# Kernel tuning notes

Hardware: AMD Instinct MI355X
Metric: run time of the kernel (lower is better)

## Reference

```python
import jax, jax.numpy as jnp
import numpy as np

B, N, FIN = 64, 128, 768
NFEAT, NHID, NHEADS, NCLASS = 1024, 512, 8, 512
ALPHA = 0.2
NEG_E = -9e15
NEG_S = -9e10


def setup_inputs():
    rng = np.random.RandomState(0)
    x = rng.randn(B, N, FIN).astype(np.float32)
    offset_mapping = np.zeros((B, N, 2), dtype=np.int32)
    attention_mask = np.zeros((B, N), dtype=np.float32)
    tag = np.zeros((B, N), dtype=np.float32)
    for b in range(B):
        pos, k, groups = 1, 0, 0
        n_words = int(rng.randint(30, 60))
        for _ in range(n_words):
            wl = int(rng.randint(1, 4))
            if k + wl > 120:
                break
            for _t in range(wl):
                offset_mapping[b, k] = (pos, pos + 2)  # contiguous inside word
                pos += 2
                k += 1
            pos += 1  # 1-char gap => word boundary: end == next_start - 1
            groups += 1
        groups -= 1  # last word is never closed (matches torch loop semantics)
        attention_mask[b, :groups] = 1.0
        tag[b, :groups] = (rng.rand(groups) > 0.1).astype(np.float32)
        tag[b, 0] = 1.0
    adj = (rng.rand(B, N, N) < 0.3).astype(np.float32)
    adj = np.clip(adj + np.eye(N, dtype=np.float32)[None], 0.0, 1.0)
    s = 0.02
    p = {
        'Wg_w': s * rng.randn(FIN, NFEAT), 'Wg_b': np.zeros(NFEAT),
        'hW_w': s * rng.randn(NHEADS, NFEAT, NHID), 'hW_b': np.zeros((NHEADS, NHID)),
        'ha_w': s * rng.randn(NHEADS, 2 * NHID), 'ha_b': np.zeros(NHEADS),
        'oW_w': s * rng.randn(NHID * NHEADS, NCLASS), 'oW_b': np.zeros(NCLASS),
        'oa_w': s * rng.randn(2 * NCLASS), 'oa_b': np.zeros(()),
        'fin_w': s * rng.randn(NCLASS, 1), 'fin_b': np.zeros(1),
    }
    inp = {
        'x': jnp.asarray(x), 'tag': jnp.asarray(tag),
        'offset_mapping': jnp.asarray(offset_mapping),
        'attention_mask': jnp.asarray(attention_mask), 'adj': jnp.asarray(adj),
    }
    for kk, vv in p.items():
        inp[kk] = jnp.asarray(np.asarray(vv, dtype=np.float32))
    return inp


def _group_pool(x, offs):
    # Vectorized form of the offset-grouped mean pooling loop.
    zero = (offs[:, :, 0] == 0) & (offs[:, :, 1] == 0)  # padding rows
    fz = jnp.argmax(zero, axis=1)                       # first padding row (break)
    pos = jnp.arange(N)
    valid = pos[None, :] < fz[:, None]
    nxt_start = jnp.concatenate([offs[:, 1:, 0], jnp.zeros((offs.shape[0], 1), offs.dtype)], axis=1)
    boundary = valid & (offs[:, :, 1] == nxt_start - 1)
    bi = boundary.astype(jnp.int32)
    cs = jnp.cumsum(bi, axis=1)
    seg = cs - bi                 # exclusive cumsum: group id per token
    G = cs[:, -1]                 # number of closed groups per row

    def per(xb, segb, bb):
        sums = jax.ops.segment_sum(xb, segb, num_segments=N + 1)[:N]
        cnts = jax.ops.segment_sum(jnp.ones((N,), xb.dtype), segb, num_segments=N + 1)[:N]
        ends = jax.ops.segment_sum((jnp.arange(N) + 1) * bb, segb, num_segments=N + 1)[:N]
        return sums, cnts, ends

    sums, cnts, ends = jax.vmap(per)(x, seg, bi)
    g = jnp.arange(N)[None, :]
    gv = g < G[:, None]
    x_off = jnp.where(gv[..., None], sums / jnp.maximum(cnts, 1.0)[..., None], 0.0)
    starts = jnp.concatenate([jnp.zeros((offs.shape[0], 1), jnp.int32), ends[:, :-1]], axis=1)
    starts = jnp.where(gv, starts, 0)
    ends = jnp.where(gv, ends, 0)
    return x_off, jnp.stack([starts, ends], axis=-1)  # [B,N,F_in], [B,N,2]


def _expand_row(fix):
    # Flatten [start,end) ranges in order until the first [0,0] row; rest = arange.
    zr = (fix[:, 0] == 0) & (fix[:, 1] == 0)
    fz = jnp.argmax(zr)
    valid = jnp.arange(N) < fz
    lens = jnp.where(valid, fix[:, 1] - fix[:, 0], 0)
    csum = jnp.cumsum(lens)
    excl = csum - lens
    total = csum[-1]
    l = jnp.arange(N)
    k = jnp.clip(jnp.searchsorted(csum, l, side='right'), 0, N - 1)
    val = fix[k, 0] + (l - excl[k])
    return jnp.where(l < total, val, l)


def _scores(x_off, tag, attention_mask, adj, Wg_w, Wg_b, hW_w, hW_b, ha_w, ha_b, oW_w, oW_b, oa_w, oa_b, fin_w, fin_b):
    xw = x_off @ Wg_w + Wg_b                                    # [B,N,NFEAT]
    h = jnp.einsum('bnf,hfo->bhno', xw, hW_w) + hW_b[None, :, None, :]
    # e_ij = leakyrelu(a1.h_i + a2.h_j + b): decomposition of a([h_i||h_j])
    e = jax.nn.leaky_relu(
        jnp.einsum('bhno,ho->bhn', h, ha_w[:, :NHID])[:, :, :, None]
        + jnp.einsum('bhno,ho->bhn', h, ha_w[:, NHID:])[:, :, None, :]
        + ha_b[None, :, None, None], ALPHA)
    att = jax.nn.softmax(jnp.where(adj[:, None, :, :] > 0, e, NEG_E), axis=-1)
    x1 = jax.nn.elu(jnp.einsum('bhij,bhjo->bhio', att, h))
    x1 = x1.transpose(0, 2, 1, 3).reshape(x1.shape[0], N, NHEADS * NHID)
    h2 = x1 @ oW_w + oW_b
    e2 = jax.nn.leaky_relu((h2 @ oa_w[:NCLASS])[:, :, None]
                           + (h2 @ oa_w[NCLASS:])[:, None, :] + oa_b, ALPHA)
    att2 = jax.nn.softmax(jnp.where(adj > 0, e2, NEG_E), axis=-1)
    x2 = jax.nn.elu(jnp.einsum('bij,bjo->bio', att2, h2))
    logits = (x2 @ fin_w + fin_b)[..., 0]                        # [B,N]
    m = jnp.where(tag > 0, attention_mask, 0.0)
    sc = jax.nn.softmax(jnp.where(m > 0, logits * m, NEG_S), axis=1)
    summary = m.sum(axis=1)
    ii = (jnp.arange(N, 0, -1).astype(jnp.float32)[None, :] / summary[:, None]) * m
    ii = jax.nn.softmax(jnp.where(m > 0, ii, NEG_S), axis=1)
    return sc + ii


def reference(x, tag, offset_mapping, attention_mask, adj, Wg_w, Wg_b, hW_w, hW_b, ha_w, ha_b, oW_w, oW_b, oa_w, oa_b, fin_w, fin_b):
    x_off, index_group = _group_pool(x, offset_mapping)
    sc = _scores(x_off, tag, attention_mask, adj, Wg_w, Wg_b, hW_w, hW_b, ha_w, ha_b, oW_w, oW_b, oa_w, oa_b, fin_w, fin_b)
    order = jnp.argsort(-sc, axis=1)  # jax argsort is stable; matches torch stable descending
    bidx = jnp.arange(sc.shape[0])[:, None]
    fix = index_group.at[bidx, order].set(index_group)  # scatter_(dim=1) with permutation index
    return jax.vmap(_expand_row)(fix)
```

## Files before the change

### kernel.cpp

```cpp
#include <hip/hip_runtime.h>
#include <cstddef>
#include <cstdint>

#define B_ 64
#define N_ 128
#define FIN_ 768
#define NEG_E_ (-9.0e15f)
#define NEG_S_ (-9.0e10f)
#define CHUNK_ 16

typedef unsigned short u16;
typedef unsigned int u32;
typedef float f32x4 __attribute__((ext_vector_type(4)));
typedef short s16x8 __attribute__((ext_vector_type(8)));
typedef u16 u16x4 __attribute__((ext_vector_type(4)));

__device__ __forceinline__ u16 f2bf(float x) {
  u32 u = __float_as_uint(x);
  return (u16)((u + 0x7fffu + ((u >> 16) & 1u)) >> 16);
}
__device__ __forceinline__ float b2f(u16 h) {
  return __uint_as_float(((u32)h) << 16);
}

__global__ __launch_bounds__(128) void group_pool_kernel(
    const float* __restrict__ x, const int* __restrict__ offs,
    u16* __restrict__ xoh, u16* __restrict__ xol, int* __restrict__ ig)
{
  const int b = blockIdx.x;
  const int fc = blockIdx.y;
  const int tid = threadIdx.x;
  __shared__ int o0[N_], o1[N_];
  __shared__ int bnd[N_];
  __shared__ float invlen[N_];
  __shared__ int st[N_], en[N_];
  __shared__ int Gs;
  o0[tid] = offs[(b * N_ + tid) * 2 + 0];
  o1[tid] = offs[(b * N_ + tid) * 2 + 1];
  bnd[tid] = -1;
  __syncthreads();
  if (tid == 0) {
    int fz = N_;
    for (int k = 0; k < N_; ++k) { if (o0[k] == 0 && o1[k] == 0) { fz = k; break; } }
    int g = 0, prev = 0;
    for (int k = 0; k < fz; ++k) {
      int nxt = (k + 1 < N_) ? o0[k + 1] : 0;
      if (o1[k] == nxt - 1 && g < N_) {
        bnd[k] = g;
        invlen[g] = 1.0f / (float)(k + 1 - prev);
        st[g] = prev;
        en[g] = k + 1;
        prev = k + 1;
        ++g;
      }
    }
    Gs = g;
  }
  __syncthreads();
  const int G = Gs;
  const int f = fc * 128 + tid;
  const float* xb = x + (size_t)b * N_ * FIN_ + f;
  float acc = 0.0f;
  for (int k0 = 0; k0 < N_; k0 += 8) {
    float v[8];
#pragma unroll
    for (int u = 0; u < 8; ++u) v[u] = xb[(size_t)(k0 + u) * FIN_];
#pragma unroll
    for (int u = 0; u < 8; ++u) {
      acc += v[u];
      int g = bnd[k0 + u];
      if (g >= 0) {
        float mean = acc * invlen[g];
        u16 hh = f2bf(mean);
        size_t oo = ((size_t)b * N_ + g) * FIN_ + f;
        xoh[oo] = hh;
        xol[oo] = f2bf(mean - b2f(hh));
        acc = 0.0f;
      }
    }
  }
  for (int g = G; g < N_; ++g) {
    size_t oo = ((size_t)b * N_ + g) * FIN_ + f;
    xoh[oo] = 0;
    xol[oo] = 0;
  }
  if (fc == 0) {
    int g = tid;
    ig[(b * N_ + g) * 2 + 0] = (g < G) ? st[g] : 0;
    ig[(b * N_ + g) * 2 + 1] = (g < G) ? en[g] : 0;
  }
}

__global__ __launch_bounds__(256) void pack_wgT(
    const float* __restrict__ w, u16* __restrict__ th, u16* __restrict__ tl)
{
  __shared__ float t[32][33];
  const int k0 = blockIdx.x * 32, n0 = blockIdx.y * 32;
  const int r = threadIdx.x >> 3;
  const int c = (threadIdx.x & 7) * 4;
  float4 v = *(const float4*)(w + (size_t)(k0 + r) * 1024 + n0 + c);
  t[r][c] = v.x; t[r][c + 1] = v.y; t[r][c + 2] = v.z; t[r][c + 3] = v.w;
  __syncthreads();
  u16x4 hv, lv;
#pragma unroll
  for (int i = 0; i < 4; ++i) {
    float xv = t[c + i][r];
    u16 h = f2bf(xv);
    hv[i] = h; lv[i] = f2bf(xv - b2f(h));
  }
  size_t dst = (size_t)(n0 + r) * 768 + k0 + c;
  *(u16x4*)(th + dst) = hv;
  *(u16x4*)(tl + dst) = lv;
}
__global__ __launch_bounds__(256) void pack_hwT(
    const float* __restrict__ w, u16* __restrict__ th, u16* __restrict__ tl)
{
  __shared__ float t[32][33];
  const int o0 = blockIdx.x * 32, f0 = blockIdx.y * 32, hd = blockIdx.z;
  const int r = threadIdx.x >> 3;
  const int c = (threadIdx.x & 7) * 4;
  float4 v = *(const float4*)(w + ((size_t)hd * 1024 + f0 + r) * 512 + o0 + c);
  t[r][c] = v.x; t[r][c + 1] = v.y; t[r][c + 2] = v.z; t[r][c + 3] = v.w;
  __syncthreads();
  u16x4 hv, lv;
#pragma unroll
  for (int i = 0; i < 4; ++i) {
    float xv = t[c + i][r];
    u16 h = f2bf(xv);
    hv[i] = h; lv[i] = f2bf(xv - b2f(h));
  }
  size_t dst = ((size_t)hd * 512 + o0 + r) * 1024 + f0 + c;
  *(u16x4*)(th + dst) = hv;
  *(u16x4*)(tl + dst) = lv;
}
__global__ __launch_bounds__(256) void pack_owT(
    const float* __restrict__ w, u16* __restrict__ th, u16* __restrict__ tl)
{
  __shared__ float t[32][33];
  const int k0 = blockIdx.x * 32, o0 = blockIdx.y * 32;
  const int r = threadIdx.x >> 3;
  const int c = (threadIdx.x & 7) * 4;
  float4 v = *(const float4*)(w + (size_t)(k0 + r) * 512 + o0 + c);
  t[r][c] = v.x; t[r][c + 1] = v.y; t[r][c + 2] = v.z; t[r][c + 3] = v.w;
  __syncthreads();
  u16x4 hv, lv;
#pragma unroll
  for (int i = 0; i < 4; ++i) {
    float xv = t[c + i][r];
    u16 h = f2bf(xv);
    hv[i] = h; lv[i] = f2bf(xv - b2f(h));
  }
  size_t dst = (size_t)(o0 + r) * 4096 + k0 + c;
  *(u16x4*)(th + dst) = hv;
  *(u16x4*)(tl + dst) = lv;
}

__global__ __launch_bounds__(256) void mfma_split_gemm(
    const u16* __restrict__ Ah, const u16* __restrict__ Al,
    const u16* __restrict__ Bh, const u16* __restrict__ Bl,
    const float* __restrict__ bias, int bias_mode,
    u16* __restrict__ Oh, u16* __restrict__ Ol, float* __restrict__ Of,
    int out_f32, int do_elu,
    int K, int lda, int ldb,
    long long Az, long long Bz,
    int msh, long long s_mb, int nsh, long long s_nb, long long s_n,
    long long zb_s, long long zh_s, int zH)
{
  __shared__ u16 As_h[128][40];
  __shared__ u16 As_l[128][40];
  __shared__ u16 Bs_h[128][40];
  __shared__ u16 Bs_l[128][40];
  const int tid = threadIdx.x;
  const int wave = tid >> 6, lane = tid & 63;
  const int wm = (wave >> 1) * 64, wn = (wave & 1) * 64;
  const int bn = blockIdx.x * 128, bm = blockIdx.y * 128;
  const int z = blockIdx.z;
  const u16* Ahb = Ah + (long long)z * Az;
  const u16* Alb = Al + (long long)z * Az;
  const u16* Bhb = Bh + (long long)z * Bz;
  const u16* Blb = Bl + (long long)z * Bz;
  const int lm = lane & 15, lq = lane >> 4;

  const int sr = tid >> 1;
  const int sc = (tid & 1) * 16;
  const size_t ga = (size_t)(bm + sr) * lda + sc;
  const size_t gb = (size_t)(bn + sr) * ldb + sc;

  f32x4 acc[4][4];
#pragma unroll
  for (int i = 0; i < 4; ++i)
#pragma unroll
    for (int j = 0; j < 4; ++j) acc[i][j] = (f32x4){0.0f, 0.0f, 0.0f, 0.0f};

  uint4 r0, r1, r2, r3, r4, r5, r6, r7;
  r0 = *(const uint4*)(Ahb + ga);
  r1 = *(const uint4*)(Ahb + ga + 8);
  r2 = *(const uint4*)(Alb + ga);
  r3 = *(const uint4*)(Alb + ga + 8);
  r4 = *(const uint4*)(Bhb + gb);
  r5 = *(const uint4*)(Bhb + gb + 8);
  r6 = *(const uint4*)(Blb + gb);
  r7 = *(const uint4*)(Blb + gb + 8);

  for (int k0 = 0; k0 < K; k0 += 32) {
    __syncthreads();
    *(uint4*)&As_h[sr][sc] = r0;
    *(uint4*)&As_h[sr][sc + 8] = r1;
    *(uint4*)&As_l[sr][sc] = r2;
    *(uint4*)&As_l[sr][sc + 8] = r3;
    *(uint4*)&Bs_h[sr][sc] = r4;
    *(uint4*)&Bs_h[sr][sc + 8] = r5;
    *(uint4*)&Bs_l[sr][sc] = r6;
    *(uint4*)&Bs_l[sr][sc + 8] = r7;
    __syncthreads();
    int kn = k0 + 32;
    if (kn < K) {
      r0 = *(const uint4*)(Ahb + ga + kn);
      r1 = *(const uint4*)(Ahb + ga + kn + 8);
      r2 = *(const uint4*)(Alb + ga + kn);
      r3 = *(const uint4*)(Alb + ga + kn + 8);
      r4 = *(const uint4*)(Bhb + gb + kn);
      r5 = *(const uint4*)(Bhb + gb + kn + 8);
      r6 = *(const uint4*)(Blb + gb + kn);
      r7 = *(const uint4*)(Blb + gb + kn + 8);
    }
    s16x8 fa_h[4], fa_l[4], fb_h[4], fb_l[4];
#pragma unroll
    for (int t = 0; t < 4; ++t) {
      fa_h[t] = *(const s16x8*)&As_h[wm + t * 16 + lm][lq * 8];
      fa_l[t] = *(const s16x8*)&As_l[wm + t * 16 + lm][lq * 8];
      fb_h[t] = *(const s16x8*)&Bs_h[wn + t * 16 + lm][lq * 8];
      fb_l[t] = *(const s16x8*)&Bs_l[wn + t * 16 + lm][lq * 8];
    }
#pragma unroll
    for (int i = 0; i < 4; ++i)
#pragma unroll
      for (int j = 0; j < 4; ++j) {
        acc[i][j] = __builtin_amdgcn_mfma_f32_16x16x32_bf16(fa_h[i], fb_h[j], acc[i][j], 0, 0, 0);
        acc[i][j] = __builtin_amdgcn_mfma_f32_16x16x32_bf16(fa_h[i], fb_l[j], acc[i][j], 0, 0, 0);
        acc[i][j] = __builtin_amdgcn_mfma_f32_16x16x32_bf16(fa_l[i], fb_h[j], acc[i][j], 0, 0, 0);
      }
  }

  __syncthreads();
  const long long zoff = (long long)(z / zH) * zb_s + (long long)(z % zH) * zh_s;
  const int mmask = (1 << msh) - 1;
  const int nmask = (1 << nsh) - 1;
  char* lds_raw = (char*)&As_h[0][0] + wave * 4608;
  const int rn = lane >> 2;
  const int rm = (lane & 3) * 16;

  if (out_f32) {
    float* slab = (float*)lds_raw;
#pragma unroll
    for (int j = 0; j < 4; ++j) {
#pragma unroll
      for (int i = 0; i < 4; ++i) {
        int mb = bm + wm + i * 16 + lq * 4;
        int n = bn + wn + j * 16 + lm;
        f32x4 v = acc[i][j];
        if (bias_mode == 1) v += bias[n];
        else if (bias_mode == 2) { f32x4 b4 = *(const f32x4*)&bias[mb]; v += b4; }
        if (do_elu) {
          v.x = v.x > 0.0f ? v.x : expm1f(v.x);
          v.y = v.y > 0.0f ? v.y : expm1f(v.y);
          v.z = v.z > 0.0f ? v.z : expm1f(v.z);
          v.w = v.w > 0.0f ? v.w : expm1f(v.w);
        }
        *(f32x4*)&slab[lm * 68 + i * 16 + lq * 4] = v;
      }
      __syncthreads();
      int n = bn + wn + j * 16 + rn;
      int mbase = bm + wm + rm;
      long long off = (long long)(mbase >> msh) * s_mb + (mbase & mmask)
                    + (long long)(n >> nsh) * s_nb + (long long)(n & nmask) * s_n + zoff;
      const float* src = &slab[rn * 68 + rm];
      f32x4 v0 = *(const f32x4*)(src + 0);
      f32x4 v1 = *(const f32x4*)(src + 4);
      f32x4 v2 = *(const f32x4*)(src + 8);
      f32x4 v3 = *(const f32x4*)(src + 12);
      *(f32x4*)(Of + off + 0)  = v0;
      *(f32x4*)(Of + off + 4)  = v1;
      *(f32x4*)(Of + off + 8)  = v2;
      *(f32x4*)(Of + off + 12) = v3;
      __syncthreads();
    }
  } else {
    u16* slab_h = (u16*)lds_raw;
    u16* slab_l = slab_h + 16 * 72;
#pragma unroll
    for (int j = 0; j < 4; ++j) {
#pragma unroll
      for (int i = 0; i < 4; ++i) {
        int mb = bm + wm + i * 16 + lq * 4;
        int n = bn + wn + j * 16 + lm;
        f32x4 v = acc[i][j];
        if (bias_mode == 1) v += bias[n];
        else if (bias_mode == 2) { f32x4 b4 = *(const f32x4*)&bias[mb]; v += b4; }
        if (do_elu) {
          v.x = v.x > 0.0f ? v.x : expm1f(v.x);
          v.y = v.y > 0.0f ? v.y : expm1f(v.y);
          v.z = v.z > 0.0f ? v.z : expm1f(v.z);
          v.w = v.w > 0.0f ? v.w : expm1f(v.w);
        }
        u16 h0 = f2bf(v.x), h1 = f2bf(v.y), h2 = f2bf(v.z), h3 = f2bf(v.w);
        u16x4 hv = {h0, h1, h2, h3};
        u16x4 lv = {f2bf(v.x - b2f(h0)), f2bf(v.y - b2f(h1)),
                    f2bf(v.z - b2f(h2)), f2bf(v.w - b2f(h3))};
        *(u16x4*)&slab_h[lm * 72 + i * 16 + lq * 4] = hv;
        *(u16x4*)&slab_l[lm * 72 + i * 16 + lq * 4] = lv;
      }
      __syncthreads();
      int n = bn + wn + j * 16 + rn;
      int mbase = bm + wm + rm;
      long long off = (long long)(mbase >> msh) * s_mb + (mbase & mmask)
                    + (long long)(n >> nsh) * s_nb + (long long)(n & nmask) * s_n + zoff;
      const u16* sh = &slab_h[rn * 72 + rm];
      const u16* sl = &slab_l[rn * 72 + rm];
      uint4 h0 = *(const uint4*)(sh + 0);
      uint4 h1 = *(const uint4*)(sh + 8);
      uint4 l0 = *(const uint4*)(sl + 0);
      uint4 l1 = *(const uint4*)(sl + 8);
      *(uint4*)(Oh + off + 0) = h0;
      *(uint4*)(Oh + off + 8) = h1;
      *(uint4*)(Ol + off + 0) = l0;
      *(uint4*)(Ol + off + 8) = l1;
      __syncthreads();
    }
  }
}

#define G8_BUF 49152

#define STAGE_A8(T) do { const int _t = (T); if (_t < nt) {                    \
    const int _q = _t % 3;                                                     \
    _Pragma("unroll")                                                          \
    for (int rg_ = 0; rg_ < 2; ++rg_)                                          \
      __builtin_amdgcn_global_load_lds(                                        \
          (const __attribute__((address_space(1))) void*)(gA +                 \
              (size_t)_t * 32 + (size_t)rg_ * 8 * lda),                        \
          (__attribute__((address_space(3))) void*)(ldsAd + _q * G8_BUF +      \
              rg_ * 1024),                                                     \
          16, 0, 0);                                                           \
  } } while (0)

#define STAGE_B8(T) do { const int _t = (T); if (_t < nt) {                    \
    const int _q = _t % 3;                                                     \
    _Pragma("unroll")                                                          \
    for (int rg_ = 0; rg_ < 4; ++rg_)                                          \
      __builtin_amdgcn_global_load_lds(                                        \
          (const __attribute__((address_space(1))) void*)(gB +                 \
              (size_t)_t * 32 + (size_t)rg_ * 8 * ldb),                        \
          (__attribute__((address_space(3))) void*)(ldsBd + _q * G8_BUF +      \
              rg_ * 1024),                                                     \
          16, 0, 0);                                                           \
  } } while (0)

__global__ __launch_bounds__(512, 2) void mfma_split_gemm8(
    const u16* __restrict__ Ah, const u16* __restrict__ Al,
    const u16* __restrict__ Bh, const u16* __restrict__ Bl,
    const float* __restrict__ bias, int bias_mode,
    u16* __restrict__ Oh, u16* __restrict__ Ol,
    int K, int lda, int ldb,
    int msh, long long s_mb, int nsh, long long s_nb, long long s_n)
{
  __shared__ __align__(128) char ldsb[3 * G8_BUF];
  const int tid = threadIdx.x;
  const int wave = tid >> 6, lane = tid & 63;
  const int wm = (wave >> 2) * 64, wn = (wave & 3) * 64;
  const int bn = blockIdx.x * 256, bm = blockIdx.y * 128;
  const int lm = lane & 15, lq = lane >> 4;
  const int nt = K >> 5;

  const int srow = lane >> 3;
  const int sl = (lane & 7) ^ srow;
  const int scol = (sl & 3) * 8;
  const u16* Asel = (sl < 4) ? Ah : Al;
  const u16* Bsel = (sl < 4) ? Bh : Bl;

  const u16* gA = Asel + (size_t)(bm + wave * 16 + srow) * lda + scol;
  const u16* gB = Bsel + (size_t)(bn + wave * 32 + srow) * ldb + scol;
  char* ldsAd = ldsb + wave * 2048;
  char* ldsBd = ldsb + 16384 + wave * 4096;

  const int hbyt = (lq ^ (lm & 7)) * 16;
  const int lbyt = hbyt ^ 64;

  f32x4 acc[4][4];
#pragma unroll
  for (int i = 0; i < 4; ++i)
#pragma unroll
    for (int j = 0; j < 4; ++j) acc[i][j] = (f32x4){0.0f, 0.0f, 0.0f, 0.0f};

  STAGE_A8(0); STAGE_B8(0);
  STAGE_A8(1); STAGE_B8(1);
  if (nt > 1) asm volatile("s_waitcnt vmcnt(6)" ::: "memory");
  else        asm volatile("s_waitcnt vmcnt(0)" ::: "memory");
  __builtin_amdgcn_s_barrier();
  __builtin_amdgcn_sched_barrier(0);

#pragma unroll 3
  for (int t = 0; t < nt; ++t) {
    const int q = t % 3;
    STAGE_A8(t + 2);
    STAGE_B8(t + 2);
    const char* Abase = ldsb + q * G8_BUF + (wm + lm) * 128;
    const char* Bbase = ldsb + q * G8_BUF + 16384 + (wn + lm) * 128;
    s16x8 fa[4][2], fb[4][2];
#pragma unroll
    for (int i = 0; i < 4; ++i) {
      fb[i][0] = *(const s16x8*)(Bbase + i * 2048 + hbyt);
      fb[i][1] = *(const s16x8*)(Bbase + i * 2048 + lbyt);
      fa[i][0] = *(const s16x8*)(Abase + i * 2048 + hbyt);
      fa[i][1] = *(const s16x8*)(Abase + i * 2048 + lbyt);
    }
    __builtin_amdgcn_s_setprio(1);
#pragma unroll
    for (int i = 0; i < 4; ++i)
#pragma unroll
      for (int j = 0; j < 4; ++j) {
        acc[i][j] = __builtin_amdgcn_mfma_f32_16x16x32_bf16(fa[i][0], fb[j][0], acc[i][j], 0, 0, 0);
        acc[i][j] = __builtin_amdgcn_mfma_f32_16x16x32_bf16(fa[i][0], fb[j][1], acc[i][j], 0, 0, 0);
        acc[i][j] = __builtin_amdgcn_mfma_f32_16x16x32_bf16(fa[i][1], fb[j][0], acc[i][j], 0, 0, 0);
      }
    __builtin_amdgcn_s_setprio(0);
    if (t + 1 < nt) {
      if (t + 2 < nt) asm volatile("s_waitcnt vmcnt(6)" ::: "memory");
      else            asm volatile("s_waitcnt vmcnt(0)" ::: "memory");
      __builtin_amdgcn_s_barrier();
      __builtin_amdgcn_sched_barrier(0);
    }
  }

  __syncthreads();
  const int mmask = (1 << msh) - 1;
  const int nmask = (1 << nsh) - 1;
  char* lds_raw = ldsb + wave * 4608;
  const int rn = lane >> 2;
  const int rm = (lane & 3) * 16;
  u16* slab_h = (u16*)lds_raw;
  u16* slab_l = slab_h + 16 * 72;
#pragma unroll
  for (int j = 0; j < 4; ++j) {
#pragma unroll
    for (int i = 0; i < 4; ++i) {
      int mb = bm + wm + i * 16 + lq * 4;
      int n = bn + wn + j * 16 + lm;
      f32x4 v = acc[i][j];
      if (bias_mode == 1) v += bias[n];
      else if (bias_mode == 2) { f32x4 b4 = *(const f32x4*)&bias[mb]; v += b4; }
      u16 h0 = f2bf(v.x), h1 = f2bf(v.y), h2 = f2bf(v.z), h3 = f2bf(v.w);
      u16x4 hv = {h0, h1, h2, h3};
      u16x4 lv = {f2bf(v.x - b2f(h0)), f2bf(v.y - b2f(h1)),
                  f2bf(v.z - b2f(h2)), f2bf(v.w - b2f(h3))};
      *(u16x4*)&slab_h[lm * 72 + i * 16 + lq * 4] = hv;
      *(u16x4*)&slab_l[lm * 72 + i * 16 + lq * 4] = lv;
    }
    __syncthreads();
    int n = bn + wn + j * 16 + rn;
    int mbase = bm + wm + rm;
    long long off = (long long)(mbase >> msh) * s_mb + (mbase & mmask)
                  + (long long)(n >> nsh) * s_nb + (long long)(n & nmask) * s_n;
    const u16* sh = &slab_h[rn * 72 + rm];
    const u16* slp = &slab_l[rn * 72 + rm];
    uint4 h0 = *(const uint4*)(sh + 0);
    uint4 h1 = *(const uint4*)(sh + 8);
    uint4 l0 = *(const uint4*)(slp + 0);
    uint4 l1 = *(const uint4*)(slp + 8);
    *(uint4*)(Oh + off + 0) = h0;
    *(uint4*)(Oh + off + 8) = h1;
    *(uint4*)(Ol + off + 0) = l0;
    *(uint4*)(Ol + off + 8) = l1;
    __syncthreads();
  }
}

__global__ __launch_bounds__(256) void reduce4_bias(
    const float* __restrict__ ps, const float* __restrict__ bias,
    float* __restrict__ h2T, int col0)
{
  int base = (blockIdx.x * 256 + threadIdx.x) * 4;
  int o = base >> 11, m = base & 2047;
  f32x4 v = *(const f32x4*)(ps + base);
  v += *(const f32x4*)(ps + base + 1048576);
  v += *(const f32x4*)(ps + base + 2097152);
  v += *(const f32x4*)(ps + base + 3145728);
  v += bias[o];
  *(f32x4*)(h2T + (size_t)o * 8192 + col0 + m) = v;
}

__global__ __launch_bounds__(512) void dot_pairs_hT(
    const u16* __restrict__ hTh, const u16* __restrict__ hTl,
    const float* __restrict__ W,
    float* __restrict__ esrc, float* __restrict__ edst)
{
  int bh = blockIdx.x;
  int head = bh & 7;
  int tid = threadIdx.x;
  int os = tid >> 7, i = tid & 127;
  const u16* ph = hTh + (size_t)bh * 65536 + (size_t)os * 16384 + i;
  const u16* pl = hTl + (size_t)bh * 65536 + (size_t)os * 16384 + i;
  const float* w1 = W + head * 1024 + os * 128;
  float s1 = 0.0f, s2 = 0.0f;
#pragma unroll 8
  for (int o = 0; o < 128; ++o) {
    float hv = b2f(ph[o * 128]) + b2f(pl[o * 128]);
    s1 = fmaf(hv, w1[o], s1);
    s2 = fmaf(hv, w1[512 + o], s2);
  }
  __shared__ float sh1[4][128], sh2[4][128];
  sh1[os][i] = s1;
  sh2[os][i] = s2;
  __syncthreads();
  if (os == 0) {
    esrc[bh * 128 + i] = sh1[0][i] + sh1[1][i] + sh1[2][i] + sh1[3][i];
    edst[bh * 128 + i] = sh2[0][i] + sh2[1][i] + sh2[2][i] + sh2[3][i];
  }
}

__global__ __launch_bounds__(512) void dot_pairs_h2T(
    const float* __restrict__ h2T, const float* __restrict__ oa,
    float* __restrict__ e2s, float* __restrict__ e2d)
{
  int b = blockIdx.x;
  int tid = threadIdx.x;
  int os = tid >> 7, i = tid & 127;
  const float* hb = h2T + (size_t)os * 128 * 8192 + b * 128 + i;
  const float* oa1 = oa + os * 128;
  float s1 = 0.0f, s2 = 0.0f;
#pragma unroll 8
  for (int o = 0; o < 128; ++o) {
    float hv = hb[(size_t)o * 8192];
    s1 = fmaf(hv, oa1[o], s1);
    s2 = fmaf(hv, oa1[512 + o], s2);
  }
  __shared__ float sh1[4][128], sh2[4][128];
  sh1[os][i] = s1;
  sh2[os][i] = s2;
  __syncthreads();
  if (os == 0) {
    e2s[b * 128 + i] = sh1[0][i] + sh1[1][i] + sh1[2][i] + sh1[3][i];
    e2d[b * 128 + i] = sh2[0][i] + sh2[1][i] + sh2[2][i] + sh2[3][i];
  }
}

__global__ __launch_bounds__(64) void edge_softmax_kernel(
    const float* __restrict__ esrc, const float* __restrict__ edst,
    const float* __restrict__ bias, const float* __restrict__ adj,
    float* __restrict__ attf, u16* __restrict__ atth, u16* __restrict__ attl,
    int H, int split)
{
  int row = blockIdx.x;
  int lane = threadIdx.x;
  int i = row & 127;
  int bh = row >> 7;
  int hd = bh % H;
  int b = bh / H;
  float es = esrc[row] + bias[hd];
  const float* adjr = adj + ((size_t)b * N_ + i) * N_;
  const float* edr = edst + (size_t)bh * N_;
  float v[2];
#pragma unroll
  for (int t = 0; t < 2; ++t) {
    int j = lane + t * 64;
    float e = es + edr[j];
    e = (e >= 0.0f) ? e : 0.2f * e;
    v[t] = (adjr[j] > 0.0f) ? e : NEG_E_;
  }
  float mx = fmaxf(v[0], v[1]);
  for (int off = 32; off; off >>= 1) mx = fmaxf(mx, __shfl_xor(mx, off));
  float e0 = expf(v[0] - mx), e1 = expf(v[1] - mx);
  float sm = e0 + e1;
  for (int off = 32; off; off >>= 1) sm += __shfl_xor(sm, off);
  float inv = 1.0f / sm;
  float p0 = e0 * inv, p1 = e1 * inv;
  size_t base = (size_t)row * N_;
  if (split) {
    u16 h0 = f2bf(p0), h1 = f2bf(p1);
    atth[base + lane] = h0;
    attl[base + lane] = f2bf(p0 - b2f(h0));
    atth[base + lane + 64] = h1;
    attl[base + lane + 64] = f2bf(p1 - b2f(h1));
  } else {
    attf[base + lane] = p0;
    attf[base + lane + 64] = p1;
  }
}

__global__ __launch_bounds__(256) void bgemm_elu_bt_f32(
    const float* __restrict__ A, const float* __restrict__ BT,
    float* __restrict__ C)
{
  __shared__ float As[16][64];
  __shared__ float Bs[16][68];
  const int tid = threadIdx.x;
  const int tm = blockIdx.x >> 3, tn = blockIdx.x & 7;
  const int bm = tm * 64, bn = tn * 64;
  const int b = blockIdx.y;
  const float* Ab = A + (size_t)b * 16384;
  const float* BTb = BT + (size_t)b * 128;
  const int ty = tid >> 4, tx = tid & 15;
  const int ar = tid >> 2, ac = (tid & 3) * 4;
  float acc[4][4];
#pragma unroll
  for (int i = 0; i < 4; ++i)
#pragma unroll
    for (int j = 0; j < 4; ++j) acc[i][j] = 0.0f;

  for (int k0 = 0; k0 < 128; k0 += 16) {
    float4 av = *(const float4*)(Ab + (size_t)(bm + ar) * 128 + k0 + ac);
    float4 bv = *(const float4*)(BTb + (size_t)(bn + ar) * 8192 + k0 + ac);
    __syncthreads();
    As[ac + 0][ar] = av.x; As[ac + 1][ar] = av.y; As[ac + 2][ar] = av.z; As[ac + 3][ar] = av.w;
    Bs[ac + 0][ar] = bv.x; Bs[ac + 1][ar] = bv.y; Bs[ac + 2][ar] = bv.z; Bs[ac + 3][ar] = bv.w;
    __syncthreads();
#pragma unroll
    for (int kk = 0; kk < 16; ++kk) {
      float a[4], bb[4];
      *(float4*)a  = *(const float4*)&As[kk][ty * 4];
      *(float4*)bb = *(const float4*)&Bs[kk][tx * 4];
#pragma unroll
      for (int i = 0; i < 4; ++i)
#pragma unroll
        for (int j = 0; j < 4; ++j)
          acc[i][j] = fmaf(a[i], bb[j], acc[i][j]);
    }
  }
#pragma unroll
  for (int i = 0; i < 4; ++i) {
    int row = b * 128 + bm + ty * 4 + i;
    float4 v;
    v.x = acc[i][0] > 0.0f ? acc[i][0] : expm1f(acc[i][0]);
    v.y = acc[i][1] > 0.0f ? acc[i][1] : expm1f(acc[i][1]);
    v.z = acc[i][2] > 0.0f ? acc[i][2] : expm1f(acc[i][2]);
    v.w = acc[i][3] > 0.0f ? acc[i][3] : expm1f(acc[i][3]);
    *(float4*)(C + (size_t)row * 512 + bn + tx * 4) = v;
  }
}

__global__ __launch_bounds__(256) void logits_kernel(
    const float* __restrict__ X, const float* __restrict__ w,
    const float* __restrict__ bptr, float* __restrict__ out, int R)
{
  int wv = (blockIdx.x * 256 + threadIdx.x) >> 6;
  int lane = threadIdx.x & 63;
  if (wv >= R) return;
  const float* xr = X + (size_t)wv * 512;
  float s = 0.0f;
#pragma unroll
  for (int i = 0; i < 8; ++i) {
    int c = lane + i * 64;
    s = fmaf(xr[c], w[c], s);
  }
  for (int off = 32; off; off >>= 1) s += __shfl_down(s, off);
  if (lane == 0) out[wv] = s + bptr[0];
}

__global__ __launch_bounds__(128) void finalize_kernel(
    const float* __restrict__ logits, const float* __restrict__ tag,
    const float* __restrict__ amask, const int* __restrict__ ig,
    int* __restrict__ out)
{
  const int b = blockIdx.x, tid = threadIdx.x;
  __shared__ float red[N_];
  __shared__ float scs[N_];
  __shared__ int fs[N_], fe[N_], lens[N_], csum[N_];
  __shared__ int redi[N_];

  float lg = logits[b * N_ + tid];
  float tg = tag[b * N_ + tid];
  float am = amask[b * N_ + tid];
  float m = (tg > 0.0f) ? am : 0.0f;

  float in1 = (m > 0.0f) ? lg * m : NEG_S_;
  red[tid] = in1; __syncthreads();
  for (int s = 64; s > 0; s >>= 1) { if (tid < s) red[tid] = fmaxf(red[tid], red[tid + s]); __syncthreads(); }
  float M1 = red[0]; __syncthreads();
  float e1 = expf(in1 - M1);
  red[tid] = e1; __syncthreads();
  for (int s = 64; s > 0; s >>= 1) { if (tid < s) red[tid] += red[tid + s]; __syncthreads(); }
  float S1 = red[0]; __syncthreads();
  float sc = e1 / S1;

  red[tid] = m; __syncthreads();
  for (int s = 64; s > 0; s >>= 1) { if (tid < s) red[tid] += red[tid + s]; __syncthreads(); }
  float SM = red[0]; __syncthreads();

  float in2 = (m > 0.0f) ? ((float)(N_ - tid) / SM) * m : NEG_S_;
  red[tid] = in2; __syncthreads();
  for (int s = 64; s > 0; s >>= 1) { if (tid < s) red[tid] = fmaxf(red[tid], red[tid + s]); __syncthreads(); }
  float M2 = red[0]; __syncthreads();
  float e2 = expf(in2 - M2);
  red[tid] = e2; __syncthreads();
  for (int s = 64; s > 0; s >>= 1) { if (tid < s) red[tid] += red[tid + s]; __syncthreads(); }
  float S2 = red[0]; __syncthreads();
  float ii = e2 / S2;

  scs[tid] = sc + ii;
  __syncthreads();

  float si = scs[tid];
  int rank = 0;
  for (int j = 0; j < N_; ++j) {
    float sj = scs[j];
    rank += (sj > si) || (sj == si && j < tid);
  }
  fs[tid] = ig[(b * N_ + rank) * 2 + 0];
  fe[tid] = ig[(b * N_ + rank) * 2 + 1];
  __syncthreads();

  redi[tid] = (fs[tid] == 0 && fe[tid] == 0) ? tid : N_;
  __syncthreads();
  for (int s = 64; s > 0; s >>= 1) { if (tid < s) redi[tid] = min(redi[tid], redi[tid + s]); __syncthreads(); }
  int fz = redi[0]; __syncthreads();
  lens[tid] = (tid < fz) ? (fe[tid] - fs[tid]) : 0;
  __syncthreads();
  if (tid == 0) {
    int r = 0;
    for (int k = 0; k < N_; ++k) { r += lens[k]; csum[k] = r; }
  }
  __syncthreads();
  int total = csum[N_ - 1];
  int l = tid;
  int k = 0;
  while (k < N_ && csum[k] <= l) ++k;
  if (k > N_ - 1) k = N_ - 1;
  int val = fs[k] + (l - (csum[k] - lens[k]));
  out[b * N_ + l] = (l < total) ? val : l;
}

extern "C" void kernel_launch(void* const* d_in, const int* in_sizes, int n_in,
                              void* d_out, int out_size, void* d_ws, size_t ws_size,
                              hipStream_t stream)
{
  const float* x     = (const float*)d_in[0];
  const float* tag   = (const float*)d_in[1];
  const int*   offs  = (const int*)  d_in[2];
  const float* amask = (const float*)d_in[3];
  const float* adj   = (const float*)d_in[4];
  const float* Wg_w  = (const float*)d_in[5];
  const float* Wg_b  = (const float*)d_in[6];
  const float* hW_w  = (const float*)d_in[7];
  const float* hW_b  = (const float*)d_in[8];
  const float* ha_w  = (const float*)d_in[9];
  const float* ha_b  = (const float*)d_in[10];
  const float* oW_w  = (const float*)d_in[11];
  const float* oW_b  = (const float*)d_in[12];
  const float* oa_w  = (const float*)d_in[13];
  const float* oa_b  = (const float*)d_in[14];
  const float* fin_w = (const float*)d_in[15];
  const float* fin_b = (const float*)d_in[16];
  int* out = (int*)d_out;

  char* ws = (char*)d_ws;
  size_t o = 0;
  int* ig     = (int*)(ws + o);  o += 131072;
  u16* WgT_h  = (u16*)(ws + o);  o += 1572864;
  u16* WgT_l  = (u16*)(ws + o);  o += 1572864;
  u16* hWT_h  = (u16*)(ws + o);  o += 8388608;
  u16* hWT_l  = (u16*)(ws + o);  o += 8388608;
  u16* oWT_h  = (u16*)(ws + o);  o += 4194304;
  u16* oWT_l  = (u16*)(ws + o);  o += 4194304;
  float* h2T  = (float*)(ws + o); o += 16777216;
  float* esrc = (float*)(ws + o); o += 65536;
  float* edst = (float*)(ws + o); o += 65536;
  float* e2s  = (float*)(ws + o); o += 32768;
  float* e2d  = (float*)(ws + o); o += 32768;
  float* lgts = (float*)(ws + o); o += 32768;
  u16* xw_h   = (u16*)(ws + o);  o += 16777216;
  u16* xw_l   = (u16*)(ws + o);  o += 16777216;
  char* pool  = ws + o;          o += 75497472;

  u16* xoff_h = (u16*)(pool + 0);
  u16* xoff_l = (u16*)(pool + 12582912);
  u16* hT_h   = (u16*)(pool + 0);
  u16* hT_l   = (u16*)(pool + 16777216);
  u16* x1_h   = (u16*)(pool + 33554432);
  u16* x1_l   = (u16*)(pool + 50331648);
  u16* att_h  = (u16*)(pool + 67108864);
  u16* att_l  = (u16*)(pool + 71303168);
  float* ps   = (float*)(pool + 0);
  float* att2 = (float*)(pool + 0);
  float* x2   = (float*)(pool + 4194304);

  pack_wgT<<<dim3(24, 32), 256, 0, stream>>>(Wg_w, WgT_h, WgT_l);
  pack_hwT<<<dim3(16, 32, 8), 256, 0, stream>>>(hW_w, hWT_h, hWT_l);
  pack_owT<<<dim3(128, 16), 256, 0, stream>>>(oW_w, oWT_h, oWT_l);

  group_pool_kernel<<<dim3(B_, 6), 128, 0, stream>>>(x, offs, xoff_h, xoff_l, ig);

  mfma_split_gemm8<<<dim3(32, 8), 512, 0, stream>>>(
      WgT_h, WgT_l, xoff_h, xoff_l, Wg_b, 2,
      xw_h, xw_l,
      768, 768, 768,
      10, 0, 13, 0, 1024);

  for (int b0 = 0; b0 < B_; b0 += CHUNK_) {
    mfma_split_gemm8<<<dim3(16, 16), 512, 0, stream>>>(
        xw_h + (size_t)b0 * 131072, xw_l + (size_t)b0 * 131072,
        hWT_h, hWT_l, hW_b, 1,
        hT_h, hT_l,
        1024, 1024, 1024,
        7, 524288, 9, 65536, 128);

    dot_pairs_hT<<<CHUNK_ * 8, 512, 0, stream>>>(hT_h, hT_l, ha_w, esrc, edst);
    edge_softmax_kernel<<<CHUNK_ * 8 * 128, 64, 0, stream>>>(
        esrc, edst, ha_b, adj + (size_t)b0 * 16384, nullptr, att_h, att_l, 8, 1);

    mfma_split_gemm<<<dim3(1, 4, CHUNK_ * 8), 256, 0, stream>>>(
        hT_h, hT_l, att_h, att_l, nullptr, 0,
        x1_h, x1_l, nullptr, 0, 1,
        128, 128, 128, 65536, 16384,
        9, 0, 7, 0, 4096, 524288, 512, 8);

    mfma_split_gemm<<<dim3(4, 16, 4), 256, 0, stream>>>(
        x1_h, x1_l, oWT_h, oWT_l, nullptr, 0,
        nullptr, nullptr, ps, 1, 0,
        1024, 4096, 4096, 1024, 1024,
        13, 0, 9, 0, 2048, 0, 1048576, 4);
    reduce4_bias<<<1024, 256, 0, stream>>>(ps, oW_b, h2T, b0 * 128);
  }

  dot_pairs_h2T<<<64, 512, 0, stream>>>(h2T, oa_w, e2s, e2d);
  edge_softmax_kernel<<<8192, 64, 0, stream>>>(e2s, e2d, oa_b, adj,
      att2, nullptr, nullptr, 1, 0);
  bgemm_elu_bt_f32<<<dim3(16, 64), 256, 0, stream>>>(att2, h2T, x2);

  logits_kernel<<<2048, 256, 0, stream>>>(x2, fin_w, fin_b, lgts, 8192);
  finalize_kernel<<<B_, 128, 0, stream>>>(lgts, tag, amask, ig, out);
}
```

Baseline: 831.1 us.

## Parallelize group-pool boundary detection with prefix scan and per-group threads

Replaces the single-thread serial scan that finds word boundaries with a parallel atomicMin plus a Hillis-Steele prefix sum over 128 tokens. The pooling loop now assigns each group to a thread slice: 256 threads each handle two features, iterating over a group's token range with float2 loads and writing packed bf16 hi/lo pairs. This removes the serial prologue and the sequential dependence through all 128 rows, at the cost of more syncthreads and uneven work across groups. The group_pool kernel is small relative to the whole pipeline.

```diff
diff --git a/kernel.cpp b/kernel.cpp
--- a/kernel.cpp
+++ b/kernel.cpp
@@ -14,6 +14,7 @@
 typedef float f32x4 __attribute__((ext_vector_type(4)));
 typedef short s16x8 __attribute__((ext_vector_type(8)));
 typedef u16 u16x4 __attribute__((ext_vector_type(4)));
+typedef u16 u16x2 __attribute__((ext_vector_type(2)));
 
 __device__ __forceinline__ u16 f2bf(float x) {
   u32 u = __float_as_uint(x);
@@ -23,71 +24,76 @@
   return __uint_as_float(((u32)h) << 16);
 }
 
-__global__ __launch_bounds__(128) void group_pool_kernel(
+__global__ __launch_bounds__(256) void group_pool_kernel(
     const float* __restrict__ x, const int* __restrict__ offs,
     u16* __restrict__ xoh, u16* __restrict__ xol, int* __restrict__ ig)
 {
   const int b = blockIdx.x;
   const int fc = blockIdx.y;
   const int tid = threadIdx.x;
-  __shared__ int o0[N_], o1[N_];
-  __shared__ int bnd[N_];
+  __shared__ int o0[N_ + 1], o1[N_];
+  __shared__ int bi[N_], cs[N_];
+  __shared__ int st[N_], en[N_];
   __shared__ float invlen[N_];
-  __shared__ int st[N_], en[N_];
-  __shared__ int Gs;
-  o0[tid] = offs[(b * N_ + tid) * 2 + 0];
-  o1[tid] = offs[(b * N_ + tid) * 2 + 1];
-  bnd[tid] = -1;
-  __syncthreads();
-  if (tid == 0) {
-    int fz = N_;
-    for (int k = 0; k < N_; ++k) { if (o0[k] == 0 && o1[k] == 0) { fz = k; break; } }
-    int g = 0, prev = 0;
-    for (int k = 0; k < fz; ++k) {
-      int nxt = (k + 1 < N_) ? o0[k + 1] : 0;
-      if (o1[k] == nxt - 1 && g < N_) {
-        bnd[k] = g;
-        invlen[g] = 1.0f / (float)(k + 1 - prev);
-        st[g] = prev;
-        en[g] = k + 1;
-        prev = k + 1;
-        ++g;
-      }
-    }
-    Gs = g;
-  }
-  __syncthreads();
-  const int G = Gs;
-  const int f = fc * 128 + tid;
-  const float* xb = x + (size_t)b * N_ * FIN_ + f;
-  float acc = 0.0f;
-  for (int k0 = 0; k0 < N_; k0 += 8) {
-    float v[8];
-#pragma unroll
-    for (int u = 0; u < 8; ++u) v[u] = xb[(size_t)(k0 + u) * FIN_];
-#pragma unroll
-    for (int u = 0; u < 8; ++u) {
-      acc += v[u];
-      int g = bnd[k0 + u];
-      if (g >= 0) {
-        float mean = acc * invlen[g];
-        u16 hh = f2bf(mean);
-        size_t oo = ((size_t)b * N_ + g) * FIN_ + f;
-        xoh[oo] = hh;
-        xol[oo] = f2bf(mean - b2f(hh));
-        acc = 0.0f;
-      }
-    }
-  }
-  for (int g = G; g < N_; ++g) {
-    size_t oo = ((size_t)b * N_ + g) * FIN_ + f;
-    xoh[oo] = 0;
-    xol[oo] = 0;
-  }
-  if (fc == 0) {
+  __shared__ int fzs;
+
+  if (tid < N_) {
+    o0[tid] = offs[(b * N_ + tid) * 2 + 0];
+    o1[tid] = offs[(b * N_ + tid) * 2 + 1];
+  }
+  if (tid == 0) { o0[N_] = 0; fzs = N_; }
+  __syncthreads();
+  if (tid < N_ && o0[tid] == 0 && o1[tid] == 0) atomicMin(&fzs, tid);
+  __syncthreads();
+  const int fz = fzs;
+  if (tid < N_) {
+    int nxt = o0[tid + 1];
+    bi[tid] = (tid < fz && o1[tid] == nxt - 1) ? 1 : 0;
+    cs[tid] = bi[tid];
+  }
+  __syncthreads();
+  for (int d = 1; d < N_; d <<= 1) {
+    int v = 0;
+    if (tid < N_ && tid >= d) v = cs[tid - d];
+    __syncthreads();
+    if (tid < N_) cs[tid] += v;
+    __syncthreads();
+  }
+  if (tid < N_ && bi[tid]) en[cs[tid] - 1] = tid + 1;
+  __syncthreads();
+  const int G = cs[N_ - 1];
+  if (tid < G) {
+    int s = tid ? en[tid - 1] : 0;
+    st[tid] = s;
+    invlen[tid] = 1.0f / (float)(en[tid] - s);
+  }
+  __syncthreads();
+  if (fc == 0 && tid < N_) {
     int g = tid;
     ig[(b * N_ + g) * 2 + 0] = (g < G) ? st[g] : 0;
     ig[(b * N_ + g) * 2 + 1] = (g < G) ? en[g] : 0;
+  }
+
+  const int f = fc * 128 + (tid & 63) * 2;
+  const float* xb = x + (size_t)b * N_ * FIN_ + f;
+  for (int g = tid >> 6; g < N_; g += 4) {
+    u16 h0 = 0, h1 = 0, l0 = 0, l1 = 0;
+    if (g < G) {
+      int s = st[g], e = en[g];
+      float s0 = 0.0f, s1 = 0.0f;
+      for (int k = s; k < e; ++k) {
+        float2 v = *(const float2*)(xb + (size_t)k * FIN_);
+        s0 += v.x; s1 += v.y;
+      }
+      float il = invlen[g];
+      float m0 = s0 * il, m1 = s1 * il;
+      h0 = f2bf(m0); l0 = f2bf(m0 - b2f(h0));
+      h1 = f2bf(m1); l1 = f2bf(m1 - b2f(h1));
+    }
+    size_t oo = ((size_t)b * N_ + g) * FIN_ + f;
+    u16x2 hv = {h0, h1}, lv = {l0, l1};
+    *(u16x2*)(xoh + oo) = hv;
+    *(u16x2*)(xol + oo) = lv;
   }
 }
 
@@ -787,7 +793,7 @@
   pack_hwT<<<dim3(16, 32, 8), 256, 0, stream>>>(hW_w, hWT_h, hWT_l);
   pack_owT<<<dim3(128, 16), 256, 0, stream>>>(oW_w, oWT_h, oWT_l);
 
-  group_pool_kernel<<<dim3(B_, 6), 128, 0, stream>>>(x, offs, xoff_h, xoff_l, ig);
+  group_pool_kernel<<<dim3(B_, 6), 256, 0, stream>>>(x, offs, xoff_h, xoff_l, ig);
 
   mfma_split_gemm8<<<dim3(32, 8), 512, 0, stream>>>(
       WgT_h, WgT_l, xoff_h, xoff_l, Wg_b, 2,
```

Measured after the change: 802.1 us. 3.5% less time.
